# Kernel optimization log

Hardware: AMD Instinct MI355X
Metric: run time of the kernel (lower is better)

Reference implementation:

```python
import jax, jax.numpy as jnp
import numpy as np

EPS = 1e-5  # torch LayerNorm default eps
L2_EPS = 1e-12


def _l2norm(t, axis=-1):
    return t / jnp.sqrt(jnp.sum(t * t, axis=axis, keepdims=True) + L2_EPS)


def setup_inputs() -> dict:
    key = jax.random.key(0)
    k1, k2, k3 = jax.random.split(key, 3)
    b, n, d = 4, 2048, 1024
    h, e, cs = 8, 16, 2048
    x = jax.random.normal(k1, (b, n, d), dtype=jnp.float32)
    # xavier_normal_ on [h, d, e]: fan_in = d*e, fan_out = h*e
    std = float(np.sqrt(2.0 / (d * e + h * e)))
    rand_projs = jax.random.normal(k2, (h, d, e), dtype=jnp.float32) * std
    codebook = jax.random.normal(k3, (h, cs, e), dtype=jnp.float32)
    return {"x": x, "rand_projs": rand_projs, "codebook": codebook}


def reference(x, rand_projs, codebook):
    # LayerNorm over last dim, no affine
    mu = jnp.mean(x, axis=-1, keepdims=True)
    var = jnp.mean((x - mu) ** 2, axis=-1, keepdims=True)
    xn = (x - mu) / jnp.sqrt(var + EPS)
    # per-head random projection: [b,n,d] x [h,d,e] -> [b,n,h,e]
    proj = jnp.einsum('bnd,hde->bnhe', xn, rand_projs)
    # cosine-sim VQ per head: normalize both, argmax similarity
    q = _l2norm(proj, axis=-1)                 # [b,n,h,e]
    cb = _l2norm(codebook, axis=-1)            # [h,c,e]
    sim = jnp.einsum('bnhe,hce->bnhc', q, cb)  # [b,n,h,c]
    indices = jnp.argmax(sim, axis=-1)         # [b,n,h] int
    return indices
```

## Files before the change

kernel.cpp:

```cpp
#include <hip/hip_runtime.h>
#include <math.h>


typedef short bf16x8 __attribute__((ext_vector_type(8)));
typedef float f32x4 __attribute__((ext_vector_type(4)));

__device__ __forceinline__ void stage16(const float* g, float* lds_base) {
  __builtin_amdgcn_global_load_lds(
      (const __attribute__((address_space(1))) void*)g,
      (__attribute__((address_space(3))) void*)lds_base, 16, 0, 0);
}

__device__ __forceinline__ unsigned short f2bf(float f) {
  unsigned u = __builtin_bit_cast(unsigned, f);
  unsigned r = (u + 0x7FFFu + ((u >> 16) & 1u)) >> 16;
  return (unsigned short)r;
}
__device__ __forceinline__ float bf2f(unsigned short b) {
  return __builtin_bit_cast(float, (unsigned)b << 16);
}
__device__ __forceinline__ void split3(float v, unsigned short& h,
                                       unsigned short& m, unsigned short& l) {
  h = f2bf(v);
  float r = v - bf2f(h);
  m = f2bf(r);
  float r2 = r - bf2f(m);
  l = f2bf(r2);
}

__global__ __launch_bounds__(256) void k_prep(const float* __restrict__ cb,
                                              const float* __restrict__ W,
                                              unsigned short* __restrict__ cfrag,
                                              float* __restrict__ csum,
                                              unsigned short* __restrict__ wfrag) {
  __shared__ float red[16][17];
  const int bid = blockIdx.x;
  const int t = threadIdx.x;
  if (bid < 64) {
    int v = bid * 256 + t;
    int h = v >> 11, c = v & 2047, tl = c >> 4, n = c & 15;
    const float4* p = (const float4*)(cb + (size_t)v * 16);
    float4 q0 = p[0], q1 = p[1], q2 = p[2], q3 = p[3];
    float f[16] = {q0.x,q0.y,q0.z,q0.w, q1.x,q1.y,q1.z,q1.w,
                   q2.x,q2.y,q2.z,q2.w, q3.x,q3.y,q3.z,q3.w};
    double s = 0.0;
#pragma unroll
    for (int i = 0; i < 16; ++i) s += (double)f[i] * (double)f[i];
    double inv = 1.0 / sqrt(s + 1e-12);
    __attribute__((aligned(16))) unsigned short vp[3][16];
#pragma unroll
    for (int i = 0; i < 16; ++i)
      split3((float)((double)f[i] * inv), vp[0][i], vp[1][i], vp[2][i]);
#pragma unroll
    for (int pp = 0; pp < 3; ++pp) {
      size_t base = ((((size_t)h * 128 + tl) * 3 + pp) * 16 + n) * 16;
      ((bf16x8*)(cfrag + base))[0] = ((bf16x8*)vp[pp])[0];
      ((bf16x8*)(cfrag + base))[1] = ((bf16x8*)vp[pp])[1];
    }
  } else if (bid < 72) {
    int h = bid - 64;
    int e = t & 15, part = t >> 4;
    const float* base = W + h * 16384 + e;
    float s = 0.f;
    int d0 = part * 64;
    for (int i = 0; i < 64; ++i) s += base[(d0 + i) * 16];
    red[e][part] = s;
    __syncthreads();
    if (t < 16) {
      float tt = 0.f;
#pragma unroll
      for (int p = 0; p < 16; ++p) tt += red[t][p];
      csum[h * 16 + t] = tt;
    }
  } else {
    int id = (bid - 72) * 256 + t;
    int o = id & 1, n = (id >> 1) & 15, c = (id >> 5) & 7, dg = id >> 8;
    __attribute__((aligned(16))) unsigned short vp[3][8];
#pragma unroll
    for (int j = 0; j < 8; ++j) {
      float v = W[c * 16384 + (dg * 16 + o * 8 + j) * 16 + n];
      split3(v, vp[0][j], vp[1][j], vp[2][j]);
    }
#pragma unroll
    for (int pp = 0; pp < 3; ++pp) {
      size_t base = ((((size_t)dg * 8 + c) * 3 + pp) * 16 + n) * 16 + o * 8;
      *(bf16x8*)(wfrag + base) = *(bf16x8*)vp[pp];
    }
  }
}

__global__ __launch_bounds__(512) void k_main(const float* __restrict__ x,
                                              const unsigned short* __restrict__ wfrag,
                                              const unsigned short* __restrict__ cfrag,
                                              const float* __restrict__ csum,
                                              int* __restrict__ out) {
  __shared__ __align__(16) float smemF[16 * 1028];
  __shared__ float sPs[8][2][16];
  __shared__ float sMu[16];
  const int t = threadIdx.x;
  const int lane = t & 63, w = t >> 6;
  const int r0 = blockIdx.x * 16;
  const int q = lane >> 4, n16 = lane & 15, oct = q & 1;
  const bool qlt2 = (q < 2);
  const int p1 = qlt2 ? 0 : 1, p2 = qlt2 ? 1 : 0, p3 = qlt2 ? 2 : 0;
  const int ehalf = oct * 8;
  unsigned short* tS = (unsigned short*)((char*)smemF + 33792);

#pragma unroll
  for (int rr = 0; rr < 2; ++rr)
#pragma unroll
    for (int j4 = 0; j4 < 4; ++j4)
      stage16(x + (size_t)(r0 + 2 * w + rr) * 1024 + j4 * 256 + lane * 4,
              smemF + (2 * w + rr) * 1028 + j4 * 256);
  __syncthreads();

  f32x4 acc[8];
#pragma unroll
  for (int h = 0; h < 8; ++h) acc[h] = (f32x4){0.f, 0.f, 0.f, 0.f};
  float ps = 0.f;

#pragma unroll 4
  for (int dg2 = 0; dg2 < 8; ++dg2) {
    const int dg = w * 8 + dg2;
    const int dq = dg * 16 + oct * 8;
    float4 xa = *(const float4*)(smemF + n16 * 1028 + dq);
    float4 xb = *(const float4*)(smemF + n16 * 1028 + dq + 4);
    float xf[8] = {xa.x, xa.y, xa.z, xa.w, xb.x, xb.y, xb.z, xb.w};
    ps += ((xf[0] + xf[1]) + (xf[2] + xf[3])) +
          ((xf[4] + xf[5]) + (xf[6] + xf[7]));
    __attribute__((aligned(16))) unsigned short s1[8], s3[8];
#pragma unroll
    for (int j = 0; j < 8; ++j) {
      unsigned short hh, mm, ll;
      split3(xf[j], hh, mm, ll);
      s1[j] = qlt2 ? hh : mm;
      s3[j] = qlt2 ? hh : ll;
    }
    bf16x8 a1 = *(bf16x8*)s1;
    bf16x8 a3 = *(bf16x8*)s3;
#pragma unroll
    for (int hh = 0; hh < 8; ++hh) {
      size_t b0 = (((size_t)(dg * 8 + hh) * 3) * 16 + n16) * 16 + oct * 8;
      bf16x8 b1 = *(const bf16x8*)(wfrag + b0 + p1 * 256);
      bf16x8 b2 = *(const bf16x8*)(wfrag + b0 + p2 * 256);
      bf16x8 b3 = *(const bf16x8*)(wfrag + b0 + p3 * 256);
      acc[hh] = __builtin_amdgcn_mfma_f32_16x16x32_bf16(a1, b1, acc[hh], 0, 0, 0);
      acc[hh] = __builtin_amdgcn_mfma_f32_16x16x32_bf16(a1, b2, acc[hh], 0, 0, 0);
      acc[hh] = __builtin_amdgcn_mfma_f32_16x16x32_bf16(a3, b3, acc[hh], 0, 0, 0);
    }
  }

  __syncthreads();
  float* sAcc = smemF;

  if (w >= 4) {
#pragma unroll
    for (int hh = 0; hh < 8; ++hh)
#pragma unroll
      for (int r = 0; r < 4; ++r)
        sAcc[((w - 4) * 64 + lane) * 33 + hh * 4 + r] = acc[hh][r];
  }
  if (q < 2) sPs[w][q][n16] = ps;
  __syncthreads();
  if (w < 4) {
#pragma unroll
    for (int hh = 0; hh < 8; ++hh)
#pragma unroll
      for (int r = 0; r < 4; ++r)
        sAcc[(w * 64 + lane) * 33 + hh * 4 + r] =
            acc[hh][r] + sAcc[(w * 64 + lane) * 33 + hh * 4 + r];
  }
  if (t < 16) {
    float s = 0.f;
#pragma unroll
    for (int w2 = 0; w2 < 8; ++w2) s += sPs[w2][0][t] + sPs[w2][1][t];
    sMu[t] = s * (1.0f / 1024.0f);
  }
  __syncthreads();

  {
    const int l = t & 63, head = t >> 6;
    const int lq = l >> 4, ln = l & 15;
    const float cs = csum[head * 16 + ln];
#pragma unroll
    for (int r = 0; r < 4; ++r) {
      const int f = head * 4 + r;
      float v = ((sAcc[(0 * 64 + l) * 33 + f] + sAcc[(1 * 64 + l) * 33 + f]) +
                 (sAcc[(2 * 64 + l) * 33 + f] + sAcc[(3 * 64 + l) * 33 + f]));
      const int row16 = lq * 4 + r;
      float tv = v - sMu[row16] * cs;
      unsigned short vh, vm, vl;
      split3(tv, vh, vm, vl);
      const int base = (row16 * 8 + head) * 16 + ln;
      tS[base] = vh;
      tS[2048 + base] = vm;
      tS[4096 + base] = vl;
    }
  }
  __syncthreads();

  {
    const int h = w;
    const int pa3 = qlt2 ? 0 : 2;
    bf16x8 a1 = *(const bf16x8*)(tS + (p1 * 2048 + (n16 * 8 + h) * 16) + ehalf);
    bf16x8 a3 = *(const bf16x8*)(tS + (pa3 * 2048 + (n16 * 8 + h) * 16) + ehalf);

    float best[4];
    int   bidx[4];
#pragma unroll
    for (int r = 0; r < 4; ++r) { best[r] = -3.402823466e38f; bidx[r] = 0; }

#pragma unroll 4
    for (int tile = 0; tile < 128; ++tile) {
      size_t b0 = (((size_t)(h * 128 + tile) * 3) * 16 + n16) * 16 + ehalf;
      bf16x8 b1 = *(const bf16x8*)(cfrag + b0 + p1 * 256);
      bf16x8 b2 = *(const bf16x8*)(cfrag + b0 + p2 * 256);
      bf16x8 b3 = *(const bf16x8*)(cfrag + b0 + p3 * 256);
      f32x4 a = {0.f, 0.f, 0.f, 0.f};
      a = __builtin_amdgcn_mfma_f32_16x16x32_bf16(a1, b1, a, 0, 0, 0);
      a = __builtin_amdgcn_mfma_f32_16x16x32_bf16(a1, b2, a, 0, 0, 0);
      a = __builtin_amdgcn_mfma_f32_16x16x32_bf16(a3, b3, a, 0, 0, 0);
      const int code = tile * 16 + n16;
#pragma unroll
      for (int r = 0; r < 4; ++r)
        if (a[r] > best[r]) { best[r] = a[r]; bidx[r] = code; }
    }

#pragma unroll
    for (int off = 8; off >= 1; off >>= 1) {
#pragma unroll
      for (int r = 0; r < 4; ++r) {
        float ov = __shfl_xor(best[r], off, 16);
        int   oi = __shfl_xor(bidx[r], off, 16);
        if (ov > best[r] || (ov == best[r] && oi < bidx[r])) {
          best[r] = ov; bidx[r] = oi;
        }
      }
    }
    if (n16 == 0) {
#pragma unroll
      for (int r = 0; r < 4; ++r)
        out[(size_t)(r0 + q * 4 + r) * 8 + h] = bidx[r];
    }
  }
}

extern "C" void kernel_launch(void* const* d_in, const int* in_sizes, int n_in,
                              void* d_out, int out_size, void* d_ws, size_t ws_size,
                              hipStream_t stream) {
  (void)in_sizes; (void)n_in; (void)out_size; (void)ws_size;
  const float* x  = (const float*)d_in[0];
  const float* rp = (const float*)d_in[1];
  const float* cb = (const float*)d_in[2];
  int* out = (int*)d_out;

  float* ws = (float*)d_ws;
  float*          csum  = ws;
  unsigned short* wfrag = (unsigned short*)(ws + 128);
  unsigned short* cfrag = (unsigned short*)(ws + 196736);

  hipLaunchKernelGGL(k_prep, dim3(136), dim3(256), 0, stream,
                     cb, rp, cfrag, csum, wfrag);
  hipLaunchKernelGGL(k_main, dim3(512), dim3(512), 0, stream,
                     x, wfrag, cfrag, csum, out);
}
```

Baseline: 155.6 us.

## Stage x rows in two half-width chunks to shrink LDS footprint

```diff
diff --git a/kernel.cpp b/kernel.cpp
--- a/kernel.cpp
+++ b/kernel.cpp
@@ -89,12 +89,12 @@
   }
 }
 
-__global__ __launch_bounds__(512) void k_main(const float* __restrict__ x,
-                                              const unsigned short* __restrict__ wfrag,
-                                              const unsigned short* __restrict__ cfrag,
-                                              const float* __restrict__ csum,
-                                              int* __restrict__ out) {
-  __shared__ __align__(16) float smemF[16 * 1028];
+__global__ __launch_bounds__(512) void k_main(
+    const float* __restrict__ x, const unsigned short* __restrict__ wfrag,
+    const unsigned short* __restrict__ cfrag, const float* __restrict__ csum,
+    int* __restrict__ out) {
+  __shared__ __align__(16) float xbuf[16 * 548];
+  __shared__ __align__(16) unsigned short tS[6144];
   __shared__ float sPs[8][2][16];
   __shared__ float sMu[16];
   const int t = threadIdx.x;
@@ -104,54 +104,58 @@
   const bool qlt2 = (q < 2);
   const int p1 = qlt2 ? 0 : 1, p2 = qlt2 ? 1 : 0, p3 = qlt2 ? 2 : 0;
   const int ehalf = oct * 8;
-  unsigned short* tS = (unsigned short*)((char*)smemF + 33792);
-
-#pragma unroll
-  for (int rr = 0; rr < 2; ++rr)
-#pragma unroll
-    for (int j4 = 0; j4 < 4; ++j4)
-      stage16(x + (size_t)(r0 + 2 * w + rr) * 1024 + j4 * 256 + lane * 4,
-              smemF + (2 * w + rr) * 1028 + j4 * 256);
-  __syncthreads();
 
   f32x4 acc[8];
 #pragma unroll
   for (int h = 0; h < 8; ++h) acc[h] = (f32x4){0.f, 0.f, 0.f, 0.f};
   float ps = 0.f;
 
-#pragma unroll 4
-  for (int dg2 = 0; dg2 < 8; ++dg2) {
-    const int dg = w * 8 + dg2;
-    const int dq = dg * 16 + oct * 8;
-    float4 xa = *(const float4*)(smemF + n16 * 1028 + dq);
-    float4 xb = *(const float4*)(smemF + n16 * 1028 + dq + 4);
-    float xf[8] = {xa.x, xa.y, xa.z, xa.w, xb.x, xb.y, xb.z, xb.w};
-    ps += ((xf[0] + xf[1]) + (xf[2] + xf[3])) +
-          ((xf[4] + xf[5]) + (xf[6] + xf[7]));
-    __attribute__((aligned(16))) unsigned short s1[8], s3[8];
-#pragma unroll
-    for (int j = 0; j < 8; ++j) {
-      unsigned short hh, mm, ll;
-      split3(xf[j], hh, mm, ll);
-      s1[j] = qlt2 ? hh : mm;
-      s3[j] = qlt2 ? hh : ll;
-    }
-    bf16x8 a1 = *(bf16x8*)s1;
-    bf16x8 a3 = *(bf16x8*)s3;
-#pragma unroll
-    for (int hh = 0; hh < 8; ++hh) {
-      size_t b0 = (((size_t)(dg * 8 + hh) * 3) * 16 + n16) * 16 + oct * 8;
-      bf16x8 b1 = *(const bf16x8*)(wfrag + b0 + p1 * 256);
-      bf16x8 b2 = *(const bf16x8*)(wfrag + b0 + p2 * 256);
-      bf16x8 b3 = *(const bf16x8*)(wfrag + b0 + p3 * 256);
-      acc[hh] = __builtin_amdgcn_mfma_f32_16x16x32_bf16(a1, b1, acc[hh], 0, 0, 0);
-      acc[hh] = __builtin_amdgcn_mfma_f32_16x16x32_bf16(a1, b2, acc[hh], 0, 0, 0);
-      acc[hh] = __builtin_amdgcn_mfma_f32_16x16x32_bf16(a3, b3, acc[hh], 0, 0, 0);
-    }
-  }
-
-  __syncthreads();
-  float* sAcc = smemF;
+  for (int c = 0; c < 2; ++c) {
+    __syncthreads();
+#pragma unroll
+    for (int rr = 0; rr < 2; ++rr)
+#pragma unroll
+      for (int j = 0; j < 2; ++j)
+        stage16(x + (size_t)(r0 + 2 * w + rr) * 1024 + c * 512 + j * 256 + lane * 4,
+                xbuf + (2 * w + rr) * 548 + j * 256);
+    __syncthreads();
+
+#pragma unroll
+    for (int dg2 = 0; dg2 < 4; ++dg2) {
+      const int dgl = w * 4 + dg2;
+      const int dg = c * 32 + dgl;
+      const int dql = dgl * 16 + oct * 8;
+      float4 xa = *(const float4*)(xbuf + n16 * 548 + dql);
+      float4 xb = *(const float4*)(xbuf + n16 * 548 + dql + 4);
+      float xf[8] = {xa.x, xa.y, xa.z, xa.w, xb.x, xb.y, xb.z, xb.w};
+      ps += ((xf[0] + xf[1]) + (xf[2] + xf[3])) +
+            ((xf[4] + xf[5]) + (xf[6] + xf[7]));
+      __attribute__((aligned(16))) unsigned short s1[8], s3[8];
+#pragma unroll
+      for (int j = 0; j < 8; ++j) {
+        unsigned short hh, mm, ll;
+        split3(xf[j], hh, mm, ll);
+        s1[j] = qlt2 ? hh : mm;
+        s3[j] = qlt2 ? hh : ll;
+      }
+      bf16x8 a1 = *(bf16x8*)s1;
+      bf16x8 a3 = *(bf16x8*)s3;
+#pragma unroll
+      for (int hh = 0; hh < 8; ++hh) {
+        size_t b0 = (((size_t)(dg * 8 + hh) * 3) * 16 + n16) * 16 + oct * 8;
+        bf16x8 b1 = *(const bf16x8*)(wfrag + b0 + p1 * 256);
+        bf16x8 b2 = *(const bf16x8*)(wfrag + b0 + p2 * 256);
+        bf16x8 b3 = *(const bf16x8*)(wfrag + b0 + p3 * 256);
+        acc[hh] = __builtin_amdgcn_mfma_f32_16x16x32_bf16(a1, b1, acc[hh], 0, 0, 0);
+        acc[hh] = __builtin_amdgcn_mfma_f32_16x16x32_bf16(a1, b2, acc[hh], 0, 0, 0);
+        acc[hh] = __builtin_amdgcn_mfma_f32_16x16x32_bf16(a3, b3, acc[hh], 0, 0, 0);
+      }
+    }
+  }
+
+  if (q < 2) sPs[w][q][n16] = ps;
+  __syncthreads();
+  float* sAcc = xbuf;
 
   if (w >= 4) {
 #pragma unroll
@@ -160,7 +164,6 @@
       for (int r = 0; r < 4; ++r)
         sAcc[((w - 4) * 64 + lane) * 33 + hh * 4 + r] = acc[hh][r];
   }
-  if (q < 2) sPs[w][q][n16] = ps;
   __syncthreads();
   if (w < 4) {
 #pragma unroll
```

Measured after the change: 159.4 us. 2.4% more time.
